# Optimization experiments

Measured on AMD Instinct MI355X. Metric: run time of the kernel, lower is better.

Reference implementation:

```python
import jax, jax.numpy as jnp
import numpy as np

N_QUBITS = 8
N_LAYERS = 1
B = 32768
SQRT2 = float(np.sqrt(2.0))

H_GATE = jnp.array([[1.0, 1.0], [1.0, -1.0]], jnp.complex64) / SQRT2
X_GATE = jnp.array([[0.0, 1.0], [1.0, 0.0]], jnp.complex64)


def _ry(t):
    # RY(t) = [[cos(t/2), -sin(t/2)], [sin(t/2), cos(t/2)]]; supports scalar or batched t
    t = jnp.asarray(t, jnp.float32)
    c = jnp.cos(0.5 * t).astype(jnp.complex64)
    s = jnp.sin(0.5 * t).astype(jnp.complex64)
    return jnp.stack([jnp.stack([c, -s], -1), jnp.stack([s, c], -1)], -2)


def _rz(t):
    # RZ(t) = diag(exp(-i t/2), exp(+i t/2))
    t = jnp.asarray(t, jnp.float32)
    e = jnp.exp(-0.5j * t.astype(jnp.complex64))
    z = jnp.zeros_like(e)
    return jnp.stack([jnp.stack([e, z], -1), jnp.stack([z, jnp.conj(e)], -1)], -2)


def apply_1q(state, U, q):
    # state: (B, 2,...,2) with wire q at axis q+1. U: (2,2) shared or (B,2,2) per-sample.
    ax = q + 1
    s = jnp.moveaxis(state, ax, -1)
    if U.ndim == 2:
        s = jnp.einsum('...j,ij->...i', s, U)
    else:
        s = jnp.einsum('b...j,bij->b...i', s, U)
    return jnp.moveaxis(s, -1, ax)


def apply_ctrl(state, U, c, t):
    # controlled-U: apply U on target wire t where control wire c == 1
    ax_c = c + 1
    s0 = jnp.take(state, 0, axis=ax_c)
    s1 = jnp.take(state, 1, axis=ax_c)
    # after removing control axis, wire t sits at axis t+1 if t<c else axis t
    q = t if t < c else t - 1
    s1 = apply_1q(s1, U, q)
    return jnp.stack([s0, s1], axis=ax_c)


def _circuit(inputs, weights):
    b = inputs.shape[0]
    state = jnp.zeros((b,) + (2,) * N_QUBITS, jnp.complex64)
    state = state.at[(slice(None),) + (0,) * N_QUBITS].set(1.0 + 0.0j)
    # embedding: H then RY(inputs[:, q]) on every qubit
    for q in range(N_QUBITS):
        state = apply_1q(state, H_GATE, q)
        state = apply_1q(state, _ry(inputs[:, q]), q)
    # (control, target) pairs exactly as in conv_circuit_1 for n_qubits=8
    pairs = [(i, (i + 1) % 4) for i in range(4)] \
        + [(i, i + 1) for i in range(3, 7)] \
        + [(7, 3)]
    for layer in range(N_LAYERS):
        w = weights[layer]
        p = 0
        for (c, t) in pairs:
            state = apply_1q(state, _rz(w[p]), t)
            state = apply_ctrl(state, _rz(w[p + 1]), c, t)
            state = apply_1q(state, _ry(w[p + 2]), t)
            state = apply_ctrl(state, X_GATE, c, t)
            state = apply_1q(state, _ry(w[p + 3]), t)
            state = apply_ctrl(state, _rz(w[p + 4]), c, t)
            p += 5
    # probs over wires [3,4,5,6,7]: marginalize wires 0,1,2 (axes 1,2,3)
    probs = (state.real ** 2 + state.imag ** 2).sum(axis=(1, 2, 3))
    return probs.reshape(b, 32)


def setup_inputs() -> dict:
    key = jax.random.key(0)
    k1, k2 = jax.random.split(key)
    inputs = jax.random.normal(k1, (B, N_QUBITS), jnp.float32)
    weights = jax.random.uniform(k2, (N_LAYERS, (N_QUBITS + 1) * 5), jnp.float32,
                                 minval=0.0, maxval=2.0 * float(np.pi))
    return {"inputs": inputs, "weights": weights}


def reference(inputs, weights):
    return _circuit(inputs, weights)
```

## Files before the change

### kernel.cpp

```cpp
#include <hip/hip_runtime.h>

typedef __fp16 h2 __attribute__((ext_vector_type(2)));
#define HALF_INV2PI 0.07957747154594766788f

__device__ __forceinline__ h2 hpk(float lo, float hi) {
  return __builtin_amdgcn_cvt_pkrtz(lo, hi);
}
__device__ __forceinline__ h2 hsp(float a) {
  return __builtin_amdgcn_cvt_pkrtz(a, a);
}
__device__ __forceinline__ h2 hmul(h2 a, h2 b) {
  h2 d; asm("v_pk_mul_f16 %0, %1, %2" : "=v"(d) : "v"(a), "v"(b)); return d;
}
__device__ __forceinline__ h2 hfma(h2 a, h2 b, h2 c) {
  h2 d; asm("v_pk_fma_f16 %0, %1, %2, %3" : "=v"(d) : "v"(a), "v"(b), "v"(c));
  return d;
}
__device__ __forceinline__ h2 hfms(h2 a, h2 b, h2 c) {
  h2 d; asm("v_pk_fma_f16 %0, %1, %2, %3 neg_lo:[0,0,1] neg_hi:[0,0,1]"
            : "=v"(d) : "v"(a), "v"(b), "v"(c));
  return d;
}
__device__ __forceinline__ h2 hfma_sw(h2 a, h2 b, h2 c) {
  h2 d; asm("v_pk_fma_f16 %0, %1, %2, %3 op_sel:[0,1,0] op_sel_hi:[1,0,1]"
            : "=v"(d) : "v"(a), "v"(b), "v"(c));
  return d;
}
template<int CTRL>
__device__ __forceinline__ h2 hdpp(h2 v) {
  int x = __builtin_amdgcn_mov_dpp(__builtin_bit_cast(int, v), CTRL, 0xf, 0xf, true);
  return __builtin_bit_cast(h2, x);
}
__device__ __forceinline__ float hdot2(h2 a, h2 b, float c) {
#if __has_builtin(__builtin_amdgcn_fdot2)
  return __builtin_amdgcn_fdot2(a, b, c, false);
#else
  return __builtin_fmaf((float)a.y, (float)b.y,
         __builtin_fmaf((float)a.x, (float)b.x, c));
#endif
}

__device__ __forceinline__ void hw_sc(float rev, float& s, float& c) {
  s = __builtin_amdgcn_sinf(rev);
  c = __builtin_amdgcn_cosf(rev);
}

template<int J>
__device__ __forceinline__ float rl(float x) {
  return __int_as_float(__builtin_amdgcn_readlane(__float_as_int(x), J));
}
struct PC { float cB,sB,cA,sA,c0,s0,cd,sd,c4,s4; };
template<int J>
__device__ __forceinline__ PC loadpc(float cB,float sB,float cA,float sA,
                                     float c0,float s0,float cd,float sd,
                                     float c4,float s4) {
  PC c;
  c.cB=rl<J>(cB); c.sB=rl<J>(sB); c.cA=rl<J>(cA); c.sA=rl<J>(sA);
  c.c0=rl<J>(c0); c.s0=rl<J>(s0); c.cd=rl<J>(cd); c.sd=rl<J>(sd);
  c.c4=rl<J>(c4); c.s4=rl<J>(s4);
  return c;
}

#define CDIAG(s, zr, zi) do { \
    h2 _t  = hmul((zi), I[s]); \
    h2 _nR = hfms((zr), R[s], _t); \
    I[s] = hfma((zi), R[s], hmul((zr), I[s])); \
    R[s] = _nR; } while (0)

__global__ __launch_bounds__(256, 6) void qnn_main(const float* __restrict__ in,
                                                   const float* __restrict__ w,
                                                   float* __restrict__ out) {
  const int tid = threadIdx.x;
  const int wid = tid >> 6;
  const int lane = tid & 63;
  const int wv = blockIdx.x * 4 + wid;
  const int q3 = (lane >> 3) & 1, q6 = (lane >> 1) & 1, q5 = lane & 1;
  const int smp = ((lane >> 5) & 1) * 4 + ((lane >> 4) & 1) * 2 + ((lane >> 2) & 1);
  const float sgn3 = q3 ? 1.f : -1.f;
  const float sgn5 = q5 ? 1.f : -1.f;
  const float sgn6 = q6 ? 1.f : -1.f;

  float gcB,gsB,gcA,gsA,gc0,gs0,gcd,gsd,gc4,gs4;
  {
    const int jj = (lane < 9) ? lane : 0;
    const float* wp = w + jj * 5;
    float w0 = wp[0], w1 = wp[1], w2 = wp[2], w3 = wp[3], w4 = wp[4];
    hw_sc(w0 * HALF_INV2PI, gsB, gcB);
    hw_sc((w0 + w1) * HALF_INV2PI, gsA, gcA);
    hw_sc((w2 + w3) * HALF_INV2PI, gs0, gc0);
    hw_sc((w2 - w3) * HALF_INV2PI, gsd, gcd);
    hw_sc(w4 * HALF_INV2PI, gs4, gc4);
  }
#define LOADPC(J) loadpc<J>(gcB,gsB,gcA,gsA,gc0,gs0,gcd,gsd,gc4,gs4)

  float z[8];
  float vc7, vs7;
  h2 vq1p, mq1p;
  {
    const float* ip = in + (wv * 8 + smp) * 8;
    float4 A4 = ((const float4*)ip)[0], B4 = ((const float4*)ip)[1];
    float xs[8] = {A4.x, A4.y, A4.z, A4.w, B4.x, B4.y, B4.z, B4.w};
    float vc[8], vs[8];
#pragma unroll
    for (int q = 0; q < 8; ++q)
      hw_sc(__builtin_fmaf(xs[q], HALF_INV2PI, 0.125f), vs[q], vc[q]);
    float prodL = (q3 ? vs[3] : vc[3]) * (q5 ? vs[5] : vc[5]) * (q6 ? vs[6] : vc[6]);
    float t0 = prodL * vc[0], t1 = prodL * vs[0];
    float u[4] = {t0 * vc[2], t0 * vs[2], t1 * vc[2], t1 * vs[2]};
#pragma unroll
    for (int i = 0; i < 4; ++i) { z[i*2] = u[i]*vc[4]; z[i*2+1] = u[i]*vs[4]; }
    vc7 = vc[7]; vs7 = vs[7];
    vq1p = hpk(vc[1], vs[1]);
    mq1p = hpk(-vc[1], vs[1]);
  }

  h2 R[16], I[16];

  PC P0 = LOADPC(0);
  {
    h2 Y0 = hpk(-P0.s0, P0.s0);
    h2 X1 = hpk(P0.sd, -P0.sd);
    h2 c0v = hsp(P0.c0), cdv = hsp(P0.cd);
#pragma unroll
    for (int s = 0; s < 16; ++s) {
      const bool Q0 = (s & 8) != 0;
      float bb = z[s >> 1] * ((s & 1) ? vs7 : vc7);
      float br = bb * (Q0 ? P0.cA : P0.cB);
      float bi = bb * (Q0 ? P0.sA : P0.sB);
      h2 r = hmul(hsp(br), vq1p);
      h2 i = hmul(hsp(bi), mq1p);
      if (!Q0) {
        R[s] = hfma_sw(Y0, r, hmul(c0v, r));
        I[s] = hfma_sw(Y0, i, hmul(c0v, i));
      } else {
        R[s] = hfma_sw(cdv, r, hmul(X1, r));
        I[s] = hfma_sw(cdv, i, hmul(X1, i));
      }
    }
  }

  PC P1 = LOADPC(1);
  {
    h2 zr1p = hpk(P1.cB, P1.cA);
    h2 zi1p[2] = { hpk(-P1.sB, -P1.sA), hpk(P1.sB, P1.sA) };
    h2 zrBp[2], ziBp[2];
#pragma unroll
    for (int t = 0; t < 2; ++t) {
      float eps = t ? 1.f : -1.f;
      float zix = eps * P1.sB, ziy = eps * P1.sA;
      float zrx = __builtin_fmaf(P0.s4, zix, P0.c4 * P1.cB);
      float zry = __builtin_fmaf(-P0.s4, ziy, P0.c4 * P1.cA);
      float zibx = __builtin_fmaf(-P0.s4, P1.cB, P0.c4 * zix);
      float ziby = __builtin_fmaf(P0.s4, P1.cA, P0.c4 * ziy);
      zrBp[t] = hpk(zrx, zry); ziBp[t] = hpk(zibx, ziby);
    }
#pragma unroll
    for (int s = 0; s < 16; ++s) {
      const int Q2 = (s >> 2) & 1;
      if (s & 8) { CDIAG(s, zrBp[Q2], ziBp[Q2]); }
      else       { CDIAG(s, zr1p, zi1p[Q2]); }
    }
  }
  {
    h2 m00 = hpk(P1.c0, P1.sd), m01 = hpk(-P1.s0, P1.cd);
    h2 m10 = hpk(P1.s0, P1.cd), m11 = hpk(P1.c0, -P1.sd);
#pragma unroll
    for (int s = 0; s < 16; ++s) {
      if (s & 4) continue;
      const int a = s, c = s | 4;
      h2 t;
      t    = hfma(m01, R[c], hmul(m00, R[a]));
      R[c] = hfma(m11, R[c], hmul(m10, R[a])); R[a] = t;
      t    = hfma(m01, I[c], hmul(m00, I[a]));
      I[c] = hfma(m11, I[c], hmul(m10, I[a])); I[a] = t;
    }
  }

  PC P2 = LOADPC(2);
  {
    float wr0 = P2.cB, wi0 = sgn3 * P2.sB;
    float wr1 = P2.cA, wi1 = sgn3 * P2.sA;
    h2 zrq[2] = { hpk(wr0, __builtin_fmaf(P1.s4, wi0, P1.c4*wr0)),
                  hpk(wr1, __builtin_fmaf(-P1.s4, wi1, P1.c4*wr1)) };
    h2 ziq[2] = { hpk(wi0, __builtin_fmaf(P1.c4, wi0, -P1.s4*wr0)),
                  hpk(wi1, __builtin_fmaf(P1.c4, wi1,  P1.s4*wr1)) };
#pragma unroll
    for (int s = 0; s < 16; ++s) {
      const int Q2 = (s >> 2) & 1;
      CDIAG(s, zrq[Q2], ziq[Q2]);
    }
  }
  {
    float Y0 = q3 ? P2.s0 : -P2.s0;
    float X1 = q3 ? -P2.sd : P2.sd;
    h2 Xv[2] = { hsp(P2.c0), hsp(X1) };
    h2 Yv[2] = { hsp(Y0), hsp(P2.cd) };
#pragma unroll
    for (int s = 0; s < 16; ++s) {
      const int Q2 = (s >> 2) & 1;
      h2 o = hdpp<0x128>(R[s]); R[s] = hfma(Yv[Q2], o, hmul(Xv[Q2], R[s]));
      o = hdpp<0x128>(I[s]);    I[s] = hfma(Yv[Q2], o, hmul(Xv[Q2], I[s]));
    }
  }

  PC P3 = LOADPC(3);
  {
    float dr = q3 ? P3.cA : P3.cB;
    float di = q3 ? P3.sA : P3.sB;
    float ui = sgn3 * P2.s4;
    h2 z3r[2][2], z3i[2][2];
    z3r[0][0] = hsp(dr);  z3i[0][0] = hsp(-di);
    z3r[0][1] = hsp(dr);  z3i[0][1] = hsp(di);
    z3r[1][0] = hsp(__builtin_fmaf(ui, di, P2.c4*dr));
    z3i[1][0] = hsp(__builtin_fmaf(ui, dr, -P2.c4*di));
    z3r[1][1] = hsp(__builtin_fmaf(-ui, di, P2.c4*dr));
    z3i[1][1] = hsp(__builtin_fmaf(ui, dr,  P2.c4*di));
#pragma unroll
    for (int s = 0; s < 16; ++s) {
      const int Q2 = (s >> 2) & 1, Q0 = (s >> 3) & 1;
      CDIAG(s, z3r[Q2][Q0], z3i[Q2][Q0]);
    }
  }
  {
    float m00 = q3 ? P3.sd : P3.c0, m01 = q3 ? P3.cd : -P3.s0;
    float m10 = q3 ? P3.cd : P3.s0, m11 = q3 ? -P3.sd : P3.c0;
    h2 M00 = hsp(m00), M01 = hsp(m01), M10 = hsp(m10), M11 = hsp(m11);
#pragma unroll
    for (int s = 0; s < 8; ++s) {
      const int a = s, c = s | 8;
      h2 t;
      t    = hfma(M01, R[c], hmul(M00, R[a]));
      R[c] = hfma(M11, R[c], hmul(M10, R[a])); R[a] = t;
      t    = hfma(M01, I[c], hmul(M00, I[a]));
      I[c] = hfma(M11, I[c], hmul(M10, I[a])); I[a] = t;
    }
  }

  PC P4 = LOADPC(4);
  {
    float ar = q3 ? P3.c4 : 1.f, ai = q3 ? P3.s4 : 0.f;
    float wr = q3 ? P4.cA : P4.cB, wi = q3 ? P4.sA : P4.sB;
    float p = ar*wr, qq = ai*wi, r_ = ar*wi, t_ = ai*wr;
    h2 z4r[2][2] = {{hsp(p - qq), hsp(p + qq)}, {hsp(p + qq), hsp(p - qq)}};
    h2 z4i[2][2] = {{hsp(-r_ - t_), hsp(r_ - t_)}, {hsp(-r_ + t_), hsp(r_ + t_)}};
#pragma unroll
    for (int s = 0; s < 16; ++s) {
      const int Q0 = (s >> 3) & 1, Q4 = (s >> 1) & 1;
      CDIAG(s, z4r[Q0][Q4], z4i[Q0][Q4]);
    }
  }
  {
    float m00 = q3 ? P4.sd : P4.c0, m01 = q3 ? P4.cd : -P4.s0;
    float m10 = q3 ? P4.cd : P4.s0, m11 = q3 ? -P4.sd : P4.c0;
    h2 M00 = hsp(m00), M01 = hsp(m01), M10 = hsp(m10), M11 = hsp(m11);
#pragma unroll
    for (int s = 0; s < 16; ++s) {
      if (s & 2) continue;
      const int a = s, c = s | 2;
      h2 t;
      t    = hfma(M01, R[c], hmul(M00, R[a]));
      R[c] = hfma(M11, R[c], hmul(M10, R[a])); R[a] = t;
      t    = hfma(M01, I[c], hmul(M00, I[a]));
      I[c] = hfma(M11, I[c], hmul(M10, I[a])); I[a] = t;
    }
  }

  PC P5 = LOADPC(5);
  {
    float ur = q3 ? P4.c4 : 1.f, ui = q3 ? P4.s4 : 0.f;
    float w0r = P5.cB, w0i = sgn5 * P5.sB;
    float w1r = P5.cA, w1i = sgn5 * P5.sA;
    h2 z5r[2] = { hsp(__builtin_fmaf(ui, w0i, ur*w0r)),
                  hsp(__builtin_fmaf(-ui, w1i, ur*w1r)) };
    h2 z5i[2] = { hsp(__builtin_fmaf(-ui, w0r, ur*w0i)),
                  hsp(__builtin_fmaf(ui, w1r, ur*w1i)) };
#pragma unroll
    for (int s = 0; s < 16; ++s) {
      const int Q4 = (s >> 1) & 1;
      CDIAG(s, z5r[Q4], z5i[Q4]);
    }
  }
  {
    float Y0 = q5 ? P5.s0 : -P5.s0;
    float X1 = q5 ? -P5.sd : P5.sd;
    h2 Xv[2] = { hsp(P5.c0), hsp(X1) };
    h2 Yv[2] = { hsp(Y0), hsp(P5.cd) };
#pragma unroll
    for (int s = 0; s < 16; ++s) {
      const int Q4 = (s >> 1) & 1;
      h2 o = hdpp<0xB1>(R[s]); R[s] = hfma(Yv[Q4], o, hmul(Xv[Q4], R[s]));
      o = hdpp<0xB1>(I[s]);    I[s] = hfma(Yv[Q4], o, hmul(Xv[Q4], I[s]));
    }
  }

  PC P6 = LOADPC(6);
  {
    float wr = q5 ? P6.cA : P6.cB;
    float wi = sgn6 * (q5 ? P6.sA : P6.sB);
    float vi = sgn5 * P5.s4;
    h2 z6r[2] = { hsp(wr), hsp(__builtin_fmaf(-vi, wi, P5.c4*wr)) };
    h2 z6i[2] = { hsp(wi), hsp(__builtin_fmaf(vi, wr, P5.c4*wi)) };
#pragma unroll
    for (int s = 0; s < 16; ++s) {
      const int Q4 = (s >> 1) & 1;
      CDIAG(s, z6r[Q4], z6i[Q4]);
    }
  }
  {
    float X = q5 ? (q6 ? -P6.sd : P6.sd) : P6.c0;
    float Y = q5 ? P6.cd : (q6 ? P6.s0 : -P6.s0);
    h2 Xv = hsp(X), Yv = hsp(Y);
#pragma unroll
    for (int s = 0; s < 16; ++s) {
      h2 o = hdpp<0x4E>(R[s]); R[s] = hfma(Yv, o, hmul(Xv, R[s]));
      o = hdpp<0x4E>(I[s]);    I[s] = hfma(Yv, o, hmul(Xv, I[s]));
    }
  }

  PC P7 = LOADPC(7);
  {
    float ur = q5 ? P6.c4 : 1.f;
    float vi = sgn6 * (q5 ? P6.s4 : 0.f);
    float wr = q6 ? P7.cA : P7.cB, wi = q6 ? P7.sA : P7.sB;
    h2 z7r[2] = { hsp(__builtin_fmaf(vi, wi, ur*wr)),
                  hsp(__builtin_fmaf(-vi, wi, ur*wr)) };
    h2 z7i[2] = { hsp(__builtin_fmaf(vi, wr, -ur*wi)),
                  hsp(__builtin_fmaf(vi, wr, ur*wi)) };
#pragma unroll
    for (int s = 0; s < 16; ++s) {
      const int Q7 = s & 1;
      CDIAG(s, z7r[Q7], z7i[Q7]);
    }
  }
  {
    float m00 = q6 ? P7.sd : P7.c0, m01 = q6 ? P7.cd : -P7.s0;
    float m10 = q6 ? P7.cd : P7.s0, m11 = q6 ? -P7.sd : P7.c0;
    h2 M00 = hsp(m00), M01 = hsp(m01), M10 = hsp(m10), M11 = hsp(m11);
#pragma unroll
    for (int s = 0; s < 16; ++s) {
      if (s & 1) continue;
      const int a = s, c = s | 1;
      h2 t;
      t    = hfma(M01, R[c], hmul(M00, R[a]));
      R[c] = hfma(M11, R[c], hmul(M10, R[a])); R[a] = t;
      t    = hfma(M01, I[c], hmul(M00, I[a]));
      I[c] = hfma(M11, I[c], hmul(M10, I[a])); I[a] = t;
    }
  }

  PC P8 = LOADPC(8);
  {
    float ur = q6 ? P7.c4 : 1.f, ui = q6 ? P7.s4 : 0.f;
    float w0r = P8.cB, w0i = sgn3 * P8.sB;
    float w1r = P8.cA, w1i = sgn3 * P8.sA;
    h2 z8r[2] = { hsp(__builtin_fmaf(ui, w0i, ur*w0r)),
                  hsp(__builtin_fmaf(-ui, w1i, ur*w1r)) };
    h2 z8i[2] = { hsp(__builtin_fmaf(-ui, w0r, ur*w0i)),
                  hsp(__builtin_fmaf(ui, w1r, ur*w1i)) };
#pragma unroll
    for (int s = 0; s < 16; ++s) {
      const int Q7 = s & 1;
      CDIAG(s, z8r[Q7], z8i[Q7]);
    }
  }
  {
    float Y0 = q3 ? P8.s0 : -P8.s0;
    float X1 = q3 ? -P8.sd : P8.sd;
    h2 Xv[2] = { hsp(P8.c0), hsp(X1) };
    h2 Yv[2] = { hsp(Y0), hsp(P8.cd) };
#pragma unroll
    for (int s = 0; s < 16; ++s) {
      const int Q7 = s & 1;
      h2 o = hdpp<0x128>(R[s]); R[s] = hfma(Yv[Q7], o, hmul(Xv[Q7], R[s]));
      o = hdpp<0x128>(I[s]);    I[s] = hfma(Yv[Q7], o, hmul(Xv[Q7], I[s]));
    }
  }

  float acc[4] = {0.f, 0.f, 0.f, 0.f};
#pragma unroll
  for (int s = 0; s < 16; ++s) {
    acc[s & 3] = hdot2(R[s], R[s], acc[s & 3]);
    acc[s & 3] = hdot2(I[s], I[s], acc[s & 3]);
  }
  const int k0 = q3 * 16 + q5 * 4 + q6 * 2;
  float* ob = out + (wv * 8 + smp) * 32 + k0;
  *(float2*)(ob) = make_float2(acc[0], acc[1]);
  *(float2*)(ob + 8) = make_float2(acc[2], acc[3]);
}

extern "C" void kernel_launch(void* const* d_in, const int* in_sizes, int n_in,
                              void* d_out, int out_size, void* d_ws, size_t ws_size,
                              hipStream_t stream) {
  const float* inputs = (const float*)d_in[0];
  const float* weights = (const float*)d_in[1];
  float* out = (float*)d_out;
  const int B = in_sizes[0] / 8;

  hipLaunchKernelGGL(qnn_main, dim3(B / 32), dim3(256), 0, stream,
                     inputs, weights, out);
}
```

Before: 19.50 us.

## Distribute qubit 4 across lanes, halving per-thread state registers

Moves wire 4 from the per-thread register index into the lane index, so each wave now holds 4 samples instead of 8 and each thread keeps 8 packed-half amplitudes instead of 16. Gates on wire 4 now use ds_swizzle cross-lane exchanges, the grid is doubled, and launch bounds are raised to 8 waves per SIMD for occupancy. The aim is to cut per-thread register pressure and serial work and to expose more parallelism. The cost is twice as many threads repeating the shared setup work (input loads, sin/cos) and added LDS-path swizzle latency.

```diff
diff --git a/kernel.cpp b/kernel.cpp
--- a/kernel.cpp
+++ b/kernel.cpp
@@ -29,6 +29,11 @@
 template<int CTRL>
 __device__ __forceinline__ h2 hdpp(h2 v) {
   int x = __builtin_amdgcn_mov_dpp(__builtin_bit_cast(int, v), CTRL, 0xf, 0xf, true);
+  return __builtin_bit_cast(h2, x);
+}
+template<int OFF>
+__device__ __forceinline__ h2 hswz(h2 v) {
+  int x = __builtin_amdgcn_ds_swizzle(__builtin_bit_cast(int, v), OFF);
   return __builtin_bit_cast(h2, x);
 }
 __device__ __forceinline__ float hdot2(h2 a, h2 b, float c) {
@@ -67,16 +72,18 @@
     I[s] = hfma((zi), R[s], hmul((zr), I[s])); \
     R[s] = _nR; } while (0)
 
-__global__ __launch_bounds__(256, 6) void qnn_main(const float* __restrict__ in,
+__global__ __launch_bounds__(256, 8) void qnn_main(const float* __restrict__ in,
                                                    const float* __restrict__ w,
                                                    float* __restrict__ out) {
   const int tid = threadIdx.x;
   const int wid = tid >> 6;
   const int lane = tid & 63;
   const int wv = blockIdx.x * 4 + wid;
-  const int q3 = (lane >> 3) & 1, q6 = (lane >> 1) & 1, q5 = lane & 1;
-  const int smp = ((lane >> 5) & 1) * 4 + ((lane >> 4) & 1) * 2 + ((lane >> 2) & 1);
+  const int q4 = (lane >> 4) & 1, q3 = (lane >> 3) & 1,
+            q6 = (lane >> 1) & 1, q5 = lane & 1;
+  const int smp = ((lane >> 5) & 1) * 2 + ((lane >> 2) & 1);
   const float sgn3 = q3 ? 1.f : -1.f;
+  const float sgn4 = q4 ? 1.f : -1.f;
   const float sgn5 = q5 ? 1.f : -1.f;
   const float sgn6 = q6 ? 1.f : -1.f;
 
@@ -93,28 +100,27 @@
   }
 #define LOADPC(J) loadpc<J>(gcB,gsB,gcA,gsA,gc0,gs0,gcd,gsd,gc4,gs4)
 
-  float z[8];
-  float vc7, vs7;
+  float b[8];
   h2 vq1p, mq1p;
   {
-    const float* ip = in + (wv * 8 + smp) * 8;
+    const float* ip = in + (wv * 4 + smp) * 8;
     float4 A4 = ((const float4*)ip)[0], B4 = ((const float4*)ip)[1];
     float xs[8] = {A4.x, A4.y, A4.z, A4.w, B4.x, B4.y, B4.z, B4.w};
     float vc[8], vs[8];
 #pragma unroll
     for (int q = 0; q < 8; ++q)
       hw_sc(__builtin_fmaf(xs[q], HALF_INV2PI, 0.125f), vs[q], vc[q]);
-    float prodL = (q3 ? vs[3] : vc[3]) * (q5 ? vs[5] : vc[5]) * (q6 ? vs[6] : vc[6]);
+    float prodL = (q3 ? vs[3] : vc[3]) * (q4 ? vs[4] : vc[4]);
+    prodL *= (q5 ? vs[5] : vc[5]) * (q6 ? vs[6] : vc[6]);
     float t0 = prodL * vc[0], t1 = prodL * vs[0];
     float u[4] = {t0 * vc[2], t0 * vs[2], t1 * vc[2], t1 * vs[2]};
 #pragma unroll
-    for (int i = 0; i < 4; ++i) { z[i*2] = u[i]*vc[4]; z[i*2+1] = u[i]*vs[4]; }
-    vc7 = vc[7]; vs7 = vs[7];
+    for (int i = 0; i < 4; ++i) { b[i*2] = u[i]*vc[7]; b[i*2+1] = u[i]*vs[7]; }
     vq1p = hpk(vc[1], vs[1]);
     mq1p = hpk(-vc[1], vs[1]);
   }
 
-  h2 R[16], I[16];
+  h2 R[8], I[8];
 
   PC P0 = LOADPC(0);
   {
@@ -122,11 +128,10 @@
     h2 X1 = hpk(P0.sd, -P0.sd);
     h2 c0v = hsp(P0.c0), cdv = hsp(P0.cd);
 #pragma unroll
-    for (int s = 0; s < 16; ++s) {
-      const bool Q0 = (s & 8) != 0;
-      float bb = z[s >> 1] * ((s & 1) ? vs7 : vc7);
-      float br = bb * (Q0 ? P0.cA : P0.cB);
-      float bi = bb * (Q0 ? P0.sA : P0.sB);
+    for (int s = 0; s < 8; ++s) {
+      const bool Q0 = (s & 4) != 0;
+      float br = b[s] * (Q0 ? P0.cA : P0.cB);
+      float bi = b[s] * (Q0 ? P0.sA : P0.sB);
       h2 r = hmul(hsp(br), vq1p);
       h2 i = hmul(hsp(bi), mq1p);
       if (!Q0) {
@@ -155,9 +160,9 @@
       zrBp[t] = hpk(zrx, zry); ziBp[t] = hpk(zibx, ziby);
     }
 #pragma unroll
-    for (int s = 0; s < 16; ++s) {
-      const int Q2 = (s >> 2) & 1;
-      if (s & 8) { CDIAG(s, zrBp[Q2], ziBp[Q2]); }
+    for (int s = 0; s < 8; ++s) {
+      const int Q2 = (s >> 1) & 1;
+      if (s & 4) { CDIAG(s, zrBp[Q2], ziBp[Q2]); }
       else       { CDIAG(s, zr1p, zi1p[Q2]); }
     }
   }
@@ -165,9 +170,9 @@
     h2 m00 = hpk(P1.c0, P1.sd), m01 = hpk(-P1.s0, P1.cd);
     h2 m10 = hpk(P1.s0, P1.cd), m11 = hpk(P1.c0, -P1.sd);
 #pragma unroll
-    for (int s = 0; s < 16; ++s) {
-      if (s & 4) continue;
-      const int a = s, c = s | 4;
+    for (int s = 0; s < 8; ++s) {
+      if (s & 2) continue;
+      const int a = s, c = s | 2;
       h2 t;
       t    = hfma(m01, R[c], hmul(m00, R[a]));
       R[c] = hfma(m11, R[c], hmul(m10, R[a])); R[a] = t;
@@ -185,8 +190,8 @@
     h2 ziq[2] = { hpk(wi0, __builtin_fmaf(P1.c4, wi0, -P1.s4*wr0)),
                   hpk(wi1, __builtin_fmaf(P1.c4, wi1,  P1.s4*wr1)) };
 #pragma unroll
-    for (int s = 0; s < 16; ++s) {
-      const int Q2 = (s >> 2) & 1;
+    for (int s = 0; s < 8; ++s) {
+      const int Q2 = (s >> 1) & 1;
       CDIAG(s, zrq[Q2], ziq[Q2]);
     }
   }
@@ -196,8 +201,8 @@
     h2 Xv[2] = { hsp(P2.c0), hsp(X1) };
     h2 Yv[2] = { hsp(Y0), hsp(P2.cd) };
 #pragma unroll
-    for (int s = 0; s < 16; ++s) {
-      const int Q2 = (s >> 2) & 1;
+    for (int s = 0; s < 8; ++s) {
+      const int Q2 = (s >> 1) & 1;
       h2 o = hdpp<0x128>(R[s]); R[s] = hfma(Yv[Q2], o, hmul(Xv[Q2], R[s]));
       o = hdpp<0x128>(I[s]);    I[s] = hfma(Yv[Q2], o, hmul(Xv[Q2], I[s]));
     }
@@ -216,8 +221,8 @@
     z3r[1][1] = hsp(__builtin_fmaf(-ui, di, P2.c4*dr));
     z3i[1][1] = hsp(__builtin_fmaf(ui, dr,  P2.c4*di));
 #pragma unroll
-    for (int s = 0; s < 16; ++s) {
-      const int Q2 = (s >> 2) & 1, Q0 = (s >> 3) & 1;
+    for (int s = 0; s < 8; ++s) {
+      const int Q2 = (s >> 1) & 1, Q0 = (s >> 2) & 1;
       CDIAG(s, z3r[Q2][Q0], z3i[Q2][Q0]);
     }
   }
@@ -226,8 +231,8 @@
     float m10 = q3 ? P3.cd : P3.s0, m11 = q3 ? -P3.sd : P3.c0;
     h2 M00 = hsp(m00), M01 = hsp(m01), M10 = hsp(m10), M11 = hsp(m11);
 #pragma unroll
-    for (int s = 0; s < 8; ++s) {
-      const int a = s, c = s | 8;
+    for (int s = 0; s < 4; ++s) {
+      const int a = s, c = s | 4;
       h2 t;
       t    = hfma(M01, R[c], hmul(M00, R[a]));
       R[c] = hfma(M11, R[c], hmul(M10, R[a])); R[a] = t;
@@ -239,79 +244,67 @@
   PC P4 = LOADPC(4);
   {
     float ar = q3 ? P3.c4 : 1.f, ai = q3 ? P3.s4 : 0.f;
-    float wr = q3 ? P4.cA : P4.cB, wi = q3 ? P4.sA : P4.sB;
-    float p = ar*wr, qq = ai*wi, r_ = ar*wi, t_ = ai*wr;
-    h2 z4r[2][2] = {{hsp(p - qq), hsp(p + qq)}, {hsp(p + qq), hsp(p - qq)}};
-    h2 z4i[2][2] = {{hsp(-r_ - t_), hsp(r_ - t_)}, {hsp(-r_ + t_), hsp(r_ + t_)}};
-#pragma unroll
-    for (int s = 0; s < 16; ++s) {
-      const int Q0 = (s >> 3) & 1, Q4 = (s >> 1) & 1;
-      CDIAG(s, z4r[Q0][Q4], z4i[Q0][Q4]);
-    }
-  }
-  {
-    float m00 = q3 ? P4.sd : P4.c0, m01 = q3 ? P4.cd : -P4.s0;
-    float m10 = q3 ? P4.cd : P4.s0, m11 = q3 ? -P4.sd : P4.c0;
-    h2 M00 = hsp(m00), M01 = hsp(m01), M10 = hsp(m10), M11 = hsp(m11);
-#pragma unroll
-    for (int s = 0; s < 16; ++s) {
-      if (s & 2) continue;
-      const int a = s, c = s | 2;
-      h2 t;
-      t    = hfma(M01, R[c], hmul(M00, R[a]));
-      R[c] = hfma(M11, R[c], hmul(M10, R[a])); R[a] = t;
-      t    = hfma(M01, I[c], hmul(M00, I[a]));
-      I[c] = hfma(M11, I[c], hmul(M10, I[a])); I[a] = t;
+    float wr = q3 ? P4.cA : P4.cB;
+    float wi4 = sgn4 * (q3 ? P4.sA : P4.sB);
+    float p = ar * wr, t_ = ai * wr, r4 = ar * wi4, qq = ai * wi4;
+    h2 zr_[2] = { hsp(p + qq), hsp(p - qq) };
+    h2 zi_[2] = { hsp(r4 - t_), hsp(r4 + t_) };
+#pragma unroll
+    for (int s = 0; s < 8; ++s) {
+      const int Q0 = (s >> 2) & 1;
+      CDIAG(s, zr_[Q0], zi_[Q0]);
+    }
+  }
+  {
+    float X = q3 ? (q4 ? -P4.sd : P4.sd) : P4.c0;
+    float Y = q3 ? P4.cd : (q4 ? P4.s0 : -P4.s0);
+    h2 Xv = hsp(X), Yv = hsp(Y);
+#pragma unroll
+    for (int s = 0; s < 8; ++s) {
+      h2 o = hswz<0x401F>(R[s]); R[s] = hfma(Yv, o, hmul(Xv, R[s]));
+      o = hswz<0x401F>(I[s]);    I[s] = hfma(Yv, o, hmul(Xv, I[s]));
     }
   }
 
   PC P5 = LOADPC(5);
   {
-    float ur = q3 ? P4.c4 : 1.f, ui = q3 ? P4.s4 : 0.f;
-    float w0r = P5.cB, w0i = sgn5 * P5.sB;
-    float w1r = P5.cA, w1i = sgn5 * P5.sA;
-    h2 z5r[2] = { hsp(__builtin_fmaf(ui, w0i, ur*w0r)),
-                  hsp(__builtin_fmaf(-ui, w1i, ur*w1r)) };
-    h2 z5i[2] = { hsp(__builtin_fmaf(-ui, w0r, ur*w0i)),
-                  hsp(__builtin_fmaf(ui, w1r, ur*w1i)) };
-#pragma unroll
-    for (int s = 0; s < 16; ++s) {
-      const int Q4 = (s >> 1) & 1;
-      CDIAG(s, z5r[Q4], z5i[Q4]);
-    }
-  }
-  {
-    float Y0 = q5 ? P5.s0 : -P5.s0;
-    float X1 = q5 ? -P5.sd : P5.sd;
-    h2 Xv[2] = { hsp(P5.c0), hsp(X1) };
-    h2 Yv[2] = { hsp(Y0), hsp(P5.cd) };
-#pragma unroll
-    for (int s = 0; s < 16; ++s) {
-      const int Q4 = (s >> 1) & 1;
-      h2 o = hdpp<0xB1>(R[s]); R[s] = hfma(Yv[Q4], o, hmul(Xv[Q4], R[s]));
-      o = hdpp<0xB1>(I[s]);    I[s] = hfma(Yv[Q4], o, hmul(Xv[Q4], I[s]));
+    float ur = q3 ? P4.c4 : 1.f;
+    float ui4 = q3 ? sgn4 * P4.s4 : 0.f;
+    float wr = q4 ? P5.cA : P5.cB;
+    float wi = sgn5 * (q4 ? P5.sA : P5.sB);
+    h2 zr = hsp(__builtin_fmaf(-ui4, wi, ur * wr));
+    h2 zi = hsp(__builtin_fmaf(ui4, wr, ur * wi));
+#pragma unroll
+    for (int s = 0; s < 8; ++s) CDIAG(s, zr, zi);
+  }
+  {
+    float X = q4 ? (q5 ? -P5.sd : P5.sd) : P5.c0;
+    float Y = q4 ? P5.cd : (q5 ? P5.s0 : -P5.s0);
+    h2 Xv = hsp(X), Yv = hsp(Y);
+#pragma unroll
+    for (int s = 0; s < 8; ++s) {
+      h2 o = hdpp<0xB1>(R[s]); R[s] = hfma(Yv, o, hmul(Xv, R[s]));
+      o = hdpp<0xB1>(I[s]);    I[s] = hfma(Yv, o, hmul(Xv, I[s]));
     }
   }
 
   PC P6 = LOADPC(6);
   {
+    float ur6 = q4 ? P5.c4 : 1.f;
+    float vi6 = q4 ? sgn5 * P5.s4 : 0.f;
     float wr = q5 ? P6.cA : P6.cB;
     float wi = sgn6 * (q5 ? P6.sA : P6.sB);
-    float vi = sgn5 * P5.s4;
-    h2 z6r[2] = { hsp(wr), hsp(__builtin_fmaf(-vi, wi, P5.c4*wr)) };
-    h2 z6i[2] = { hsp(wi), hsp(__builtin_fmaf(vi, wr, P5.c4*wi)) };
-#pragma unroll
-    for (int s = 0; s < 16; ++s) {
-      const int Q4 = (s >> 1) & 1;
-      CDIAG(s, z6r[Q4], z6i[Q4]);
-    }
+    h2 zr = hsp(__builtin_fmaf(-vi6, wi, ur6 * wr));
+    h2 zi = hsp(__builtin_fmaf(vi6, wr, ur6 * wi));
+#pragma unroll
+    for (int s = 0; s < 8; ++s) CDIAG(s, zr, zi);
   }
   {
     float X = q5 ? (q6 ? -P6.sd : P6.sd) : P6.c0;
     float Y = q5 ? P6.cd : (q6 ? P6.s0 : -P6.s0);
     h2 Xv = hsp(X), Yv = hsp(Y);
 #pragma unroll
-    for (int s = 0; s < 16; ++s) {
+    for (int s = 0; s < 8; ++s) {
       h2 o = hdpp<0x4E>(R[s]); R[s] = hfma(Yv, o, hmul(Xv, R[s]));
       o = hdpp<0x4E>(I[s]);    I[s] = hfma(Yv, o, hmul(Xv, I[s]));
     }
@@ -327,7 +320,7 @@
     h2 z7i[2] = { hsp(__builtin_fmaf(vi, wr, -ur*wi)),
                   hsp(__builtin_fmaf(vi, wr, ur*wi)) };
 #pragma unroll
-    for (int s = 0; s < 16; ++s) {
+    for (int s = 0; s < 8; ++s) {
       const int Q7 = s & 1;
       CDIAG(s, z7r[Q7], z7i[Q7]);
     }
@@ -337,7 +330,7 @@
     float m10 = q6 ? P7.cd : P7.s0, m11 = q6 ? -P7.sd : P7.c0;
     h2 M00 = hsp(m00), M01 = hsp(m01), M10 = hsp(m10), M11 = hsp(m11);
 #pragma unroll
-    for (int s = 0; s < 16; ++s) {
+    for (int s = 0; s < 8; ++s) {
       if (s & 1) continue;
       const int a = s, c = s | 1;
       h2 t;
@@ -358,7 +351,7 @@
     h2 z8i[2] = { hsp(__builtin_fmaf(-ui, w0r, ur*w0i)),
                   hsp(__builtin_fmaf(ui, w1r, ur*w1i)) };
 #pragma unroll
-    for (int s = 0; s < 16; ++s) {
+    for (int s = 0; s < 8; ++s) {
       const int Q7 = s & 1;
       CDIAG(s, z8r[Q7], z8i[Q7]);
     }
@@ -369,23 +362,22 @@
     h2 Xv[2] = { hsp(P8.c0), hsp(X1) };
     h2 Yv[2] = { hsp(Y0), hsp(P8.cd) };
 #pragma unroll
-    for (int s = 0; s < 16; ++s) {
+    for (int s = 0; s < 8; ++s) {
       const int Q7 = s & 1;
       h2 o = hdpp<0x128>(R[s]); R[s] = hfma(Yv[Q7], o, hmul(Xv[Q7], R[s]));
       o = hdpp<0x128>(I[s]);    I[s] = hfma(Yv[Q7], o, hmul(Xv[Q7], I[s]));
     }
   }
 
-  float acc[4] = {0.f, 0.f, 0.f, 0.f};
-#pragma unroll
-  for (int s = 0; s < 16; ++s) {
-    acc[s & 3] = hdot2(R[s], R[s], acc[s & 3]);
-    acc[s & 3] = hdot2(I[s], I[s], acc[s & 3]);
-  }
-  const int k0 = q3 * 16 + q5 * 4 + q6 * 2;
-  float* ob = out + (wv * 8 + smp) * 32 + k0;
-  *(float2*)(ob) = make_float2(acc[0], acc[1]);
-  *(float2*)(ob + 8) = make_float2(acc[2], acc[3]);
+  float acc[2] = {0.f, 0.f};
+#pragma unroll
+  for (int s = 0; s < 8; ++s) {
+    acc[s & 1] = hdot2(R[s], R[s], acc[s & 1]);
+    acc[s & 1] = hdot2(I[s], I[s], acc[s & 1]);
+  }
+  const int k0 = q3 * 16 + q4 * 8 + q5 * 4 + q6 * 2;
+  float* ob = out + (wv * 4 + smp) * 32 + k0;
+  *(float2*)ob = make_float2(acc[0], acc[1]);
 }
 
 extern "C" void kernel_launch(void* const* d_in, const int* in_sizes, int n_in,
@@ -396,6 +388,6 @@
   float* out = (float*)d_out;
   const int B = in_sizes[0] / 8;
 
-  hipLaunchKernelGGL(qnn_main, dim3(B / 32), dim3(256), 0, stream,
+  hipLaunchKernelGGL(qnn_main, dim3(B / 16), dim3(256), 0, stream,
                      inputs, weights, out);
 }
```

After: 21.99 us. +12.8%, slower.
